# Kernel tuning notes

Hardware: AMD Instinct MI355X
Metric: run time of the kernel (lower is better)

## Reference

```python
import jax, jax.numpy as jnp
import numpy as np

N_NODES = 20000

def gcn(h, W, b, src, dst):
    # DGL GraphConv, norm='both': D_out^-1/2 on src, aggregate, D_in^-1/2 on dst, then W, b
    E = src.shape[0]
    ones = jnp.ones((E,), dtype=h.dtype)
    out_deg = jnp.clip(jax.ops.segment_sum(ones, src, N_NODES), 1.0)
    in_deg = jnp.clip(jax.ops.segment_sum(ones, dst, N_NODES), 1.0)
    dn_src = jax.lax.rsqrt(out_deg)  # [N]
    dn_dst = jax.lax.rsqrt(in_deg)
    hs = h * dn_src[None, :, None]           # [B,N,H]
    msg = hs[:, src, :]                      # [B,E,H] gather
    agg = jax.vmap(lambda m: jax.ops.segment_sum(m, dst, N_NODES))(msg)  # [B,N,H]
    agg = agg * dn_dst[None, :, None]
    return agg @ W + b

def setup_inputs() -> dict:
    key = jax.random.key(0)
    ks = jax.random.split(key, 16)
    B, N, H, I, E = 4, N_NODES, 128, 64, 320000
    inp = {
        'x': jax.random.normal(ks[0], (B, I), jnp.float32),
        'h_prev': jax.random.normal(ks[1], (B, N, H), jnp.float32),
        'c_prev': jax.random.normal(ks[2], (B, N, H), jnp.float32),
        'src': jax.random.randint(ks[3], (E,), 0, N, jnp.int32),
        'dst': jax.random.randint(ks[4], (E,), 0, N, jnp.int32),
    }
    s_in = 1.0 / np.sqrt(I)
    s_h = 1.0 / np.sqrt(H)
    inp['Wi'] = jax.random.uniform(ks[5], (I, H), jnp.float32, -s_in, s_in)
    inp['bi'] = jax.random.uniform(ks[6], (H,), jnp.float32, -s_in, s_in)
    inp['Wf'] = jax.random.uniform(ks[7], (I, H), jnp.float32, -s_in, s_in)
    inp['bf'] = jax.random.uniform(ks[8], (H,), jnp.float32, -s_in, s_in)
    inp['Wo'] = jax.random.uniform(ks[9], (I, H), jnp.float32, -s_in, s_in)
    inp['bo'] = jax.random.uniform(ks[10], (H,), jnp.float32, -s_in, s_in)
    inp['Wc'] = jax.random.uniform(ks[11], (I, H), jnp.float32, -s_in, s_in)
    inp['bc'] = jax.random.uniform(ks[12], (H,), jnp.float32, -s_in, s_in)
    inp['Wg'] = jax.random.uniform(ks[13], (H, H), jnp.float32, -s_h, s_h)
    inp['bg'] = jax.random.uniform(ks[14], (H,), jnp.float32, -s_h, s_h)
    return inp

def reference(x, h_prev, c_prev, src, dst, Wi, bi, Wf, bf, Wo, bo, Wc, bc, Wg, bg):
    # gcn_h(g, h_prev) is identical in all four gates -> compute once
    gh = gcn(h_prev, Wg, bg, src, dst)  # [B,N,H]
    i_t = jax.nn.sigmoid((x @ Wi + bi)[:, None, :] + gh)
    f_t = jax.nn.sigmoid((x @ Wf + bf)[:, None, :] + gh)
    o_t = jax.nn.sigmoid((x @ Wo + bo)[:, None, :] + gh)
    c_tilde = jnp.tanh((x @ Wc + bc)[:, None, :] + gh)
    c_t = f_t * c_prev + i_t * c_tilde
    h_t = o_t * jnp.tanh(c_t)
    return h_t, c_t
```

## Files before the change

kernel.cpp:

```cpp
#include <hip/hip_runtime.h>
#include <hip/hip_bf16.h>

#define N_NODES 20000
#define B 4
#define H 128
#define I_DIM 64
#define E_MAX 320000
#define CAP 64

__device__ int   g_cnt_dst[N_NODES];
__device__ int   g_deg_src[N_NODES];
__device__ int   g_csr[N_NODES * CAP];
__device__ float g_xg[4 * B * H];
__device__ uint2 g_hs[N_NODES * H];

__global__ __launch_bounds__(256)
void degree_kernel(const int* __restrict__ src, int E, int eb,
                   const float* __restrict__ x,
                   const float* __restrict__ Wi, const float* __restrict__ bi,
                   const float* __restrict__ Wf, const float* __restrict__ bf_,
                   const float* __restrict__ Wo, const float* __restrict__ bo,
                   const float* __restrict__ Wc, const float* __restrict__ bc) {
    int blk = blockIdx.x;
    int t = threadIdx.x;
    if (blk < eb) {
        int e = blk * 256 + t;
        if (e < E) atomicAdd(&g_deg_src[src[e]], 1);
    } else {
        int bid = blk - eb;
        int g = bid >> 1;
        int b = ((bid & 1) << 1) | (t >> 7);
        int h = t & 127;
        const float* W;
        const float* bb;
        switch (g) {
            case 0: W = Wi; bb = bi; break;
            case 1: W = Wf; bb = bf_; break;
            case 2: W = Wo; bb = bo; break;
            default: W = Wc; bb = bc; break;
        }
        float acc = bb[h];
#pragma unroll
        for (int i = 0; i < I_DIM; i++)
            acc += x[b * I_DIM + i] * W[i * H + h];
        g_xg[(g * B + b) * H + h] = acc;
    }
}

__global__ __launch_bounds__(256)
void mid_kernel(const float* __restrict__ h_prev,
                const int* __restrict__ src, const int* __restrict__ dst, int E) {
    const int PACK_BLKS = (N_NODES * H) / 256;
    int blk = blockIdx.x;
    int t = threadIdx.x;

    if (blk < PACK_BLKS) {
        int i = blk * 256 + t;
        int n = i >> 7;
        float sc = rsqrtf(fmaxf((float)g_deg_src[n], 1.0f));
        const long stride = (long)N_NODES * H;
        float v0 = h_prev[i] * sc;
        float v1 = h_prev[i + stride] * sc;
        float v2 = h_prev[i + 2 * stride] * sc;
        float v3 = h_prev[i + 3 * stride] * sc;
        __hip_bfloat162 p01 = __float22bfloat162_rn(make_float2(v0, v1));
        __hip_bfloat162 p23 = __float22bfloat162_rn(make_float2(v2, v3));
        uint2 wv;
        wv.x = *reinterpret_cast<unsigned int*>(&p01);
        wv.y = *reinterpret_cast<unsigned int*>(&p23);
        g_hs[i] = wv;
    } else {
        int e = (blk - PACK_BLKS) * 256 + t;
        if (e < E) {
            int d = dst[e];
            int slot = atomicAdd(&g_cnt_dst[d], 1);
            if (slot < CAP) g_csr[(d << 6) + slot] = src[e];
        }
    }
}

__device__ __forceinline__ float fast_sigmoid(float z) {
    return 1.f / (1.f + __expf(-z));
}
__device__ __forceinline__ float fast_tanh(float z) {
    return 1.f - 2.f / (__expf(2.f * z) + 1.f);
}

__global__ __launch_bounds__(256)
void fused_kernel(const float* __restrict__ Wg, const float* __restrict__ bg,
                  const float* __restrict__ c_prev,
                  float* __restrict__ out_h, float* __restrict__ out_c) {
    int t = threadIdx.x;
    int ni = t >> 7;
    int h = t & 127;
    int w = (t >> 6) & 1;
    int lane = t & 63;
    int n = (blockIdx.x << 1) + ni;

    int cnt = g_cnt_dst[n];
    float dd = rsqrtf(fmaxf((float)cnt, 1.0f));
    if (cnt > CAP) cnt = CAP;

    const long stride = (long)N_NODES * H;
    float cp[B];
#pragma unroll
    for (int b = 0; b < B; b++)
        cp[b] = __builtin_nontemporal_load(&c_prev[(long)b * stride + (long)n * H + h]);

    __shared__ int sbase[2][CAP];
    if (h < 64) {
        int s = g_csr[(n << 6) + (lane < cnt ? lane : 0)];
        sbase[ni][lane] = s << 7;
    }
    __syncthreads();

    float a0 = 0.f, a1 = 0.f, a2 = 0.f, a3 = 0.f;

#define ACC(wv) { \
        __hip_bfloat162 p01 = *reinterpret_cast<__hip_bfloat162*>(&(wv).x); \
        __hip_bfloat162 p23 = *reinterpret_cast<__hip_bfloat162*>(&(wv).y); \
        float2 f01 = __bfloat1622float2(p01); \
        float2 f23 = __bfloat1622float2(p23); \
        a0 += f01.x; a1 += f01.y; a2 += f23.x; a3 += f23.y; }

    const int* sb = sbase[ni];
    int j = 0;
    for (; j + 8 <= cnt; j += 8) {
        int b0 = sb[j];
        int b1 = sb[j + 1];
        int b2 = sb[j + 2];
        int b3 = sb[j + 3];
        int b4 = sb[j + 4];
        int b5 = sb[j + 5];
        int b6 = sb[j + 6];
        int b7 = sb[j + 7];
        uint2 w0 = g_hs[b0 + h];
        uint2 w1 = g_hs[b1 + h];
        uint2 w2 = g_hs[b2 + h];
        uint2 w3 = g_hs[b3 + h];
        uint2 w4 = g_hs[b4 + h];
        uint2 w5 = g_hs[b5 + h];
        uint2 w6 = g_hs[b6 + h];
        uint2 w7 = g_hs[b7 + h];
        ACC(w0); ACC(w1); ACC(w2); ACC(w3);
        ACC(w4); ACC(w5); ACC(w6); ACC(w7);
    }
    for (; j + 4 <= cnt; j += 4) {
        int b0 = sb[j];
        int b1 = sb[j + 1];
        int b2 = sb[j + 2];
        int b3 = sb[j + 3];
        uint2 w0 = g_hs[b0 + h];
        uint2 w1 = g_hs[b1 + h];
        uint2 w2 = g_hs[b2 + h];
        uint2 w3 = g_hs[b3 + h];
        ACC(w0); ACC(w1); ACC(w2); ACC(w3);
    }
    for (; j < cnt; j++) {
        uint2 wv = g_hs[sb[j] + h];
        ACC(wv);
    }
#undef ACC

    a0 *= dd; a1 *= dd; a2 *= dd; a3 *= dd;

    __shared__ float4 arow4[2][H];
    arow4[ni][h] = make_float4(a0, a1, a2, a3);
    __syncthreads();

    float g0 = 0.f, g1 = 0.f, g2 = 0.f, g3 = 0.f;

#pragma unroll 8
    for (int kk = 0; kk < 64; kk++) {
        int k = (w << 6) + kk;
        float wv = Wg[k * H + h];
        float b0 = __int_as_float(__builtin_amdgcn_readlane(__float_as_int(a0), kk));
        float b1 = __int_as_float(__builtin_amdgcn_readlane(__float_as_int(a1), kk));
        float b2 = __int_as_float(__builtin_amdgcn_readlane(__float_as_int(a2), kk));
        float b3 = __int_as_float(__builtin_amdgcn_readlane(__float_as_int(a3), kk));
        g0 += b0 * wv;
        g1 += b1 * wv;
        g2 += b2 * wv;
        g3 += b3 * wv;
    }
#pragma unroll 8
    for (int kk = 0; kk < 64; kk++) {
        int k = ((1 - w) << 6) + kk;
        float4 a = arow4[ni][k];
        float wv = Wg[k * H + h];
        g0 += a.x * wv;
        g1 += a.y * wv;
        g2 += a.z * wv;
        g3 += a.w * wv;
    }

    float bgh = bg[h];
    float gh_arr[B] = {g0 + bgh, g1 + bgh, g2 + bgh, g3 + bgh};
#pragma unroll
    for (int b = 0; b < B; b++) {
        float gh = gh_arr[b];
        float xi = g_xg[(0 * B + b) * H + h];
        float xf = g_xg[(1 * B + b) * H + h];
        float xo = g_xg[(2 * B + b) * H + h];
        float xc = g_xg[(3 * B + b) * H + h];

        float it = fast_sigmoid(xi + gh);
        float ft = fast_sigmoid(xf + gh);
        float ot = fast_sigmoid(xo + gh);
        float ct = fast_tanh(xc + gh);

        float c  = ft * cp[b] + it * ct;
        float ho = ot * fast_tanh(c);

        long idx = (long)b * stride + (long)n * H + h;
        __builtin_nontemporal_store(ho, &out_h[idx]);
        __builtin_nontemporal_store(c,  &out_c[idx]);
    }

    if (h == 0)  g_cnt_dst[n] = 0;
    if (h == 64) g_deg_src[n] = 0;
}

extern "C" void kernel_launch(void* const* d_in, const int* in_sizes, int n_in,
                              void* d_out, int out_size, void* d_ws, size_t ws_size,
                              hipStream_t stream) {
    const float* x      = (const float*)d_in[0];
    const float* h_prev = (const float*)d_in[1];
    const float* c_prev = (const float*)d_in[2];
    const int* src = (const int*)d_in[3];
    const int* dst = (const int*)d_in[4];
    const float* Wi = (const float*)d_in[5];
    const float* bi = (const float*)d_in[6];
    const float* Wf = (const float*)d_in[7];
    const float* bf_ = (const float*)d_in[8];
    const float* Wo = (const float*)d_in[9];
    const float* bo = (const float*)d_in[10];
    const float* Wc = (const float*)d_in[11];
    const float* bc = (const float*)d_in[12];
    const float* Wg = (const float*)d_in[13];
    const float* bg = (const float*)d_in[14];

    int E = in_sizes[3];
    if (E > E_MAX) E = E_MAX;
    int eb = (E + 255) / 256;
    const int PACK_BLKS = (N_NODES * H) / 256;

    degree_kernel<<<eb + 8, 256, 0, stream>>>(src, E, eb,
        x, Wi, bi, Wf, bf_, Wo, bo, Wc, bc);
    mid_kernel<<<PACK_BLKS + eb, 256, 0, stream>>>(h_prev, src, dst, E);

    float* out_h = (float*)d_out;
    float* out_c = out_h + (long)B * N_NODES * H;
    fused_kernel<<<N_NODES / 2, 256, 0, stream>>>(Wg, bg, c_prev, out_h, out_c);
}
```

Baseline: 315.3 us.

## Use bf16 MFMA for Wg projection with one wave per node and 16-byte gathers

Result: faster. 263.2 us (-16.5%).

```diff
diff --git a/kernel.cpp b/kernel.cpp
--- a/kernel.cpp
+++ b/kernel.cpp
@@ -8,11 +8,15 @@
 #define E_MAX 320000
 #define CAP 64
 
+typedef __attribute__((ext_vector_type(8))) short short8;
+typedef __attribute__((ext_vector_type(4))) float float4v;
+
 __device__ int   g_cnt_dst[N_NODES];
 __device__ int   g_deg_src[N_NODES];
 __device__ int   g_csr[N_NODES * CAP];
 __device__ float g_xg[4 * B * H];
-__device__ uint2 g_hs[N_NODES * H];
+__device__ __align__(16) uint2 g_hs[N_NODES * H];
+__device__ __align__(16) unsigned short g_wgB[H * H];
 
 __global__ __launch_bounds__(256)
 void degree_kernel(const int* __restrict__ src, int E, int eb,
@@ -20,13 +24,14 @@
                    const float* __restrict__ Wi, const float* __restrict__ bi,
                    const float* __restrict__ Wf, const float* __restrict__ bf_,
                    const float* __restrict__ Wo, const float* __restrict__ bo,
-                   const float* __restrict__ Wc, const float* __restrict__ bc) {
+                   const float* __restrict__ Wc, const float* __restrict__ bc,
+                   const float* __restrict__ Wg) {
     int blk = blockIdx.x;
     int t = threadIdx.x;
     if (blk < eb) {
         int e = blk * 256 + t;
         if (e < E) atomicAdd(&g_deg_src[src[e]], 1);
-    } else {
+    } else if (blk < eb + 8) {
         int bid = blk - eb;
         int g = bid >> 1;
         int b = ((bid & 1) << 1) | (t >> 7);
@@ -44,6 +49,18 @@
         for (int i = 0; i < I_DIM; i++)
             acc += x[b * I_DIM + i] * W[i * H + h];
         g_xg[(g * B + b) * H + h] = acc;
+    } else {
+        int i = (blk - eb - 8) * 256 + t;
+        int tn = i >> 11;
+        int rem = i & 2047;
+        int kb = rem >> 9;
+        int rem2 = rem & 511;
+        int lane = rem2 >> 3;
+        int j = rem2 & 7;
+        int k  = kb * 32 + (lane >> 4) * 8 + j;
+        int nn = tn * 16 + (lane & 15);
+        __hip_bfloat16 hv = __float2bfloat16(Wg[k * H + nn]);
+        g_wgB[i] = *reinterpret_cast<unsigned short*>(&hv);
     }
 }
 
@@ -85,45 +102,55 @@
 __device__ __forceinline__ float fast_tanh(float z) {
     return 1.f - 2.f / (__expf(2.f * z) + 1.f);
 }
+__device__ __forceinline__ unsigned pack2bf(float lo, float hi) {
+    __hip_bfloat162 p = __float22bfloat162_rn(make_float2(lo, hi));
+    return *reinterpret_cast<unsigned*>(&p);
+}
 
 __global__ __launch_bounds__(256)
-void fused_kernel(const float* __restrict__ Wg, const float* __restrict__ bg,
+void fused_kernel(const float* __restrict__ bg,
                   const float* __restrict__ c_prev,
                   float* __restrict__ out_h, float* __restrict__ out_c) {
     int t = threadIdx.x;
-    int ni = t >> 7;
-    int h = t & 127;
-    int w = (t >> 6) & 1;
+    int w = t >> 6;
     int lane = t & 63;
-    int n = (blockIdx.x << 1) + ni;
+    int n = (blockIdx.x << 2) + w;
+    const long stride = (long)N_NODES * H;
 
     int cnt = g_cnt_dst[n];
     float dd = rsqrtf(fmaxf((float)cnt, 1.0f));
     if (cnt > CAP) cnt = CAP;
 
-    const long stride = (long)N_NODES * H;
-    float cp[B];
-#pragma unroll
-    for (int b = 0; b < B; b++)
-        cp[b] = __builtin_nontemporal_load(&c_prev[(long)b * stride + (long)n * H + h]);
-
-    __shared__ int sbase[2][CAP];
-    if (h < 64) {
-        int s = g_csr[(n << 6) + (lane < cnt ? lane : 0)];
-        sbase[ni][lane] = s << 7;
-    }
-    __syncthreads();
+    __shared__ int sbase[4][64];
+    __shared__ unsigned short Atile[16][136];
+
+    sbase[w][lane] = g_csr[(n << 6) + (lane < cnt ? lane : 0)] << 6;
+
+    float cpr[2][4];
+    {
+        long ne = (long)((blockIdx.x << 2) + (lane >> 4));
+#pragma unroll
+        for (int i = 0; i < 2; i++) {
+            int h = (2 * w + i) * 16 + (lane & 15);
+#pragma unroll
+            for (int j = 0; j < 4; j++)
+                cpr[i][j] = __builtin_nontemporal_load(
+                    &c_prev[(long)j * stride + ne * H + h]);
+        }
+    }
 
     float a0 = 0.f, a1 = 0.f, a2 = 0.f, a3 = 0.f;
-
-#define ACC(wv) { \
-        __hip_bfloat162 p01 = *reinterpret_cast<__hip_bfloat162*>(&(wv).x); \
-        __hip_bfloat162 p23 = *reinterpret_cast<__hip_bfloat162*>(&(wv).y); \
-        float2 f01 = __bfloat1622float2(p01); \
-        float2 f23 = __bfloat1622float2(p23); \
-        a0 += f01.x; a1 += f01.y; a2 += f23.x; a3 += f23.y; }
-
-    const int* sb = sbase[ni];
+    float a4 = 0.f, a5 = 0.f, a6 = 0.f, a7 = 0.f;
+    const uint4* hs4 = reinterpret_cast<const uint4*>(g_hs);
+    const int* sb = sbase[w];
+
+#define ACCV(v) { \
+        __hip_bfloat162 p; float2 f; \
+        p = *reinterpret_cast<__hip_bfloat162*>(&(v).x); f = __bfloat1622float2(p); a0 += f.x; a1 += f.y; \
+        p = *reinterpret_cast<__hip_bfloat162*>(&(v).y); f = __bfloat1622float2(p); a2 += f.x; a3 += f.y; \
+        p = *reinterpret_cast<__hip_bfloat162*>(&(v).z); f = __bfloat1622float2(p); a4 += f.x; a5 += f.y; \
+        p = *reinterpret_cast<__hip_bfloat162*>(&(v).w); f = __bfloat1622float2(p); a6 += f.x; a7 += f.y; }
+
     int j = 0;
     for (; j + 8 <= cnt; j += 8) {
         int b0 = sb[j];
@@ -134,91 +161,75 @@
         int b5 = sb[j + 5];
         int b6 = sb[j + 6];
         int b7 = sb[j + 7];
-        uint2 w0 = g_hs[b0 + h];
-        uint2 w1 = g_hs[b1 + h];
-        uint2 w2 = g_hs[b2 + h];
-        uint2 w3 = g_hs[b3 + h];
-        uint2 w4 = g_hs[b4 + h];
-        uint2 w5 = g_hs[b5 + h];
-        uint2 w6 = g_hs[b6 + h];
-        uint2 w7 = g_hs[b7 + h];
-        ACC(w0); ACC(w1); ACC(w2); ACC(w3);
-        ACC(w4); ACC(w5); ACC(w6); ACC(w7);
-    }
-    for (; j + 4 <= cnt; j += 4) {
-        int b0 = sb[j];
-        int b1 = sb[j + 1];
-        int b2 = sb[j + 2];
-        int b3 = sb[j + 3];
-        uint2 w0 = g_hs[b0 + h];
-        uint2 w1 = g_hs[b1 + h];
-        uint2 w2 = g_hs[b2 + h];
-        uint2 w3 = g_hs[b3 + h];
-        ACC(w0); ACC(w1); ACC(w2); ACC(w3);
+        uint4 v0 = hs4[b0 + lane];
+        uint4 v1 = hs4[b1 + lane];
+        uint4 v2 = hs4[b2 + lane];
+        uint4 v3 = hs4[b3 + lane];
+        uint4 v4 = hs4[b4 + lane];
+        uint4 v5 = hs4[b5 + lane];
+        uint4 v6 = hs4[b6 + lane];
+        uint4 v7 = hs4[b7 + lane];
+        ACCV(v0); ACCV(v1); ACCV(v2); ACCV(v3);
+        ACCV(v4); ACCV(v5); ACCV(v6); ACCV(v7);
     }
     for (; j < cnt; j++) {
-        uint2 wv = g_hs[sb[j] + h];
-        ACC(wv);
-    }
-#undef ACC
-
-    a0 *= dd; a1 *= dd; a2 *= dd; a3 *= dd;
-
-    __shared__ float4 arow4[2][H];
-    arow4[ni][h] = make_float4(a0, a1, a2, a3);
+        uint4 v = hs4[sb[j] + lane];
+        ACCV(v);
+    }
+#undef ACCV
+
+    *reinterpret_cast<unsigned*>(&Atile[w * 4 + 0][2 * lane]) = pack2bf(a0 * dd, a4 * dd);
+    *reinterpret_cast<unsigned*>(&Atile[w * 4 + 1][2 * lane]) = pack2bf(a1 * dd, a5 * dd);
+    *reinterpret_cast<unsigned*>(&Atile[w * 4 + 2][2 * lane]) = pack2bf(a2 * dd, a6 * dd);
+    *reinterpret_cast<unsigned*>(&Atile[w * 4 + 3][2 * lane]) = pack2bf(a3 * dd, a7 * dd);
+
     __syncthreads();
 
-    float g0 = 0.f, g1 = 0.f, g2 = 0.f, g3 = 0.f;
-
-#pragma unroll 8
-    for (int kk = 0; kk < 64; kk++) {
-        int k = (w << 6) + kk;
-        float wv = Wg[k * H + h];
-        float b0 = __int_as_float(__builtin_amdgcn_readlane(__float_as_int(a0), kk));
-        float b1 = __int_as_float(__builtin_amdgcn_readlane(__float_as_int(a1), kk));
-        float b2 = __int_as_float(__builtin_amdgcn_readlane(__float_as_int(a2), kk));
-        float b3 = __int_as_float(__builtin_amdgcn_readlane(__float_as_int(a3), kk));
-        g0 += b0 * wv;
-        g1 += b1 * wv;
-        g2 += b2 * wv;
-        g3 += b3 * wv;
-    }
-#pragma unroll 8
-    for (int kk = 0; kk < 64; kk++) {
-        int k = ((1 - w) << 6) + kk;
-        float4 a = arow4[ni][k];
-        float wv = Wg[k * H + h];
-        g0 += a.x * wv;
-        g1 += a.y * wv;
-        g2 += a.z * wv;
-        g3 += a.w * wv;
-    }
-
-    float bgh = bg[h];
-    float gh_arr[B] = {g0 + bgh, g1 + bgh, g2 + bgh, g3 + bgh};
-#pragma unroll
-    for (int b = 0; b < B; b++) {
-        float gh = gh_arr[b];
-        float xi = g_xg[(0 * B + b) * H + h];
-        float xf = g_xg[(1 * B + b) * H + h];
-        float xo = g_xg[(2 * B + b) * H + h];
-        float xc = g_xg[(3 * B + b) * H + h];
-
-        float it = fast_sigmoid(xi + gh);
-        float ft = fast_sigmoid(xf + gh);
-        float ot = fast_sigmoid(xo + gh);
-        float ct = fast_tanh(xc + gh);
-
-        float c  = ft * cp[b] + it * ct;
-        float ho = ot * fast_tanh(c);
-
-        long idx = (long)b * stride + (long)n * H + h;
-        __builtin_nontemporal_store(ho, &out_h[idx]);
-        __builtin_nontemporal_store(c,  &out_c[idx]);
-    }
-
-    if (h == 0)  g_cnt_dst[n] = 0;
-    if (h == 64) g_deg_src[n] = 0;
+    if (t < 4)                 g_cnt_dst[(blockIdx.x << 2) + t] = 0;
+    else if (t >= 64 && t < 68) g_deg_src[(blockIdx.x << 2) + (t - 64)] = 0;
+
+    int arow = lane & 15;
+    int agrp = lane >> 4;
+    float4v c0 = {0.f, 0.f, 0.f, 0.f};
+    float4v c1 = {0.f, 0.f, 0.f, 0.f};
+#pragma unroll
+    for (int kb = 0; kb < 4; kb++) {
+        short8 af = *reinterpret_cast<const short8*>(&Atile[arow][kb * 32 + agrp * 8]);
+        short8 bf0 = *reinterpret_cast<const short8*>(
+            &g_wgB[(((2 * w) * 4 + kb) * 64 + lane) * 8]);
+        short8 bf1 = *reinterpret_cast<const short8*>(
+            &g_wgB[(((2 * w + 1) * 4 + kb) * 64 + lane) * 8]);
+        c0 = __builtin_amdgcn_mfma_f32_16x16x32_bf16(af, bf0, c0, 0, 0, 0);
+        c1 = __builtin_amdgcn_mfma_f32_16x16x32_bf16(af, bf1, c1, 0, 0, 0);
+    }
+
+    long ne = (long)((blockIdx.x << 2) + (lane >> 4));
+#pragma unroll
+    for (int i = 0; i < 2; i++) {
+        float4v c = i ? c1 : c0;
+        int h = (2 * w + i) * 16 + (lane & 15);
+        float bgh = bg[h];
+#pragma unroll
+        for (int jj = 0; jj < 4; jj++) {
+            float gh = c[jj] + bgh;
+            float xi = g_xg[(0 * B + jj) * H + h];
+            float xf = g_xg[(1 * B + jj) * H + h];
+            float xo = g_xg[(2 * B + jj) * H + h];
+            float xc = g_xg[(3 * B + jj) * H + h];
+
+            float it = fast_sigmoid(xi + gh);
+            float ft = fast_sigmoid(xf + gh);
+            float ot = fast_sigmoid(xo + gh);
+            float ct = fast_tanh(xc + gh);
+
+            float cc = ft * cpr[i][jj] + it * ct;
+            float ho = ot * fast_tanh(cc);
+
+            long idx = (long)jj * stride + ne * H + h;
+            __builtin_nontemporal_store(ho, &out_h[idx]);
+            __builtin_nontemporal_store(cc, &out_c[idx]);
+        }
+    }
 }
 
 extern "C" void kernel_launch(void* const* d_in, const int* in_sizes, int n_in,
@@ -245,11 +256,11 @@
     int eb = (E + 255) / 256;
     const int PACK_BLKS = (N_NODES * H) / 256;
 
-    degree_kernel<<<eb + 8, 256, 0, stream>>>(src, E, eb,
-        x, Wi, bi, Wf, bf_, Wo, bo, Wc, bc);
+    degree_kernel<<<eb + 8 + 64, 256, 0, stream>>>(src, E, eb,
+        x, Wi, bi, Wf, bf_, Wo, bo, Wc, bc, Wg);
     mid_kernel<<<PACK_BLKS + eb, 256, 0, stream>>>(h_prev, src, dst, E);
 
     float* out_h = (float*)d_out;
     float* out_c = out_h + (long)B * N_NODES * H;
-    fused_kernel<<<N_NODES / 2, 256, 0, stream>>>(Wg, bg, c_prev, out_h, out_c);
-}
+    fused_kernel<<<N_NODES / 4, 256, 0, stream>>>(bg, c_prev, out_h, out_c);
+}
```
